# Performance work log

Hardware: AMD Instinct MI355X
Metric: run time of the kernel (lower is better)

## Reference

```python
import jax, jax.numpy as jnp
import numpy as np

BETA = 0.25  # commitment weight from __init__ default
K, D = 512, 64


def setup_inputs() -> dict:
    key = jax.random.key(0)
    k1, k2 = jax.random.split(key)
    latents = jax.random.normal(k1, (32, 64, 64, 64), dtype=jnp.float32)  # [B, D, H, W]
    # nn.Embedding weight initialized uniform(-1/K, 1/K)
    emb_weight = jax.random.uniform(k2, (K, D), dtype=jnp.float32, minval=-1.0 / K, maxval=1.0 / K)
    return {"latents": latents, "emb_weight": emb_weight, "validation": 1}


def reference(latents, emb_weight, validation):
    B, Dc, H, W = latents.shape
    lat = jnp.transpose(latents, (0, 2, 3, 1))          # [B, H, W, D]
    flat = lat.reshape(-1, Dc)                           # [N, D]
    # pairwise squared distances via sum-of-squares + matmul (as in source)
    dist = (jnp.sum(flat * flat, axis=1, keepdims=True)
            + jnp.sum(emb_weight * emb_weight, axis=1)
            - 2.0 * flat @ emb_weight.T)                 # [N, K]
    inds = jnp.argmin(dist, axis=1)                      # [N]
    # one_hot @ emb_weight == gather
    q = emb_weight[inds].reshape(B, H, W, Dc)            # [B, H, W, D]
    commitment_loss = jnp.mean((jax.lax.stop_gradient(q) - lat) ** 2)
    embedding_loss = jnp.mean((q - jax.lax.stop_gradient(lat)) ** 2)
    # eloss starts at 0.0 (and stays 0 in validation), so topology terms vanish
    vq_loss = commitment_loss * BETA + embedding_loss
    # straight-through estimator
    q_st = lat + jax.lax.stop_gradient(q - lat)
    return jnp.transpose(q_st, (0, 3, 1, 2)), vq_loss
```

## Files before the change

### kernel.cpp

```cpp
#include <hip/hip_runtime.h>


typedef __bf16 bf16_t;
typedef __attribute__((ext_vector_type(8))) __bf16 bf16x8;
typedef __attribute__((ext_vector_type(16))) float floatx16;
typedef __attribute__((ext_vector_type(4))) float floatx4;

namespace {
constexpr int K    = 512;
constexpr int D    = 64;
constexpr int HW   = 4096;
constexpr int NPIX = 32 * HW;
constexpr int QOUT = NPIX * D;
constexpr int ROWB = 144;
constexpr int EXT_BYTES  = K * ROWB;
constexpr int BIAS_OFF   = EXT_BYTES;
constexpr int SMEM_BYTES = EXT_BYTES + K * 4;
constexpr int SMEM_CHUNKS = SMEM_BYTES / 1024;
}

__global__ __launch_bounds__(64) void vq_prep(const float* __restrict__ emb,
                                              char* __restrict__ ws,
                                              float* __restrict__ loss) {
    int k = blockIdx.x * 64 + threadIdx.x;
    if (k == 0) *loss = 0.0f;
    if (k >= K) return;
    const float4* row = (const float4*)(emb + k * D);
    float4 v[16];
#pragma unroll
    for (int i = 0; i < 16; ++i) v[i] = row[i];
    float s = 0.0f;
#pragma unroll
    for (int i = 0; i < 16; ++i)
        s += v[i].x * v[i].x + v[i].y * v[i].y + v[i].z * v[i].z + v[i].w * v[i].w;
    bf16_t r[72];
#pragma unroll
    for (int i = 0; i < 16; ++i) {
        r[4 * i + 0] = (bf16_t)v[i].x;
        r[4 * i + 1] = (bf16_t)v[i].y;
        r[4 * i + 2] = (bf16_t)v[i].z;
        r[4 * i + 3] = (bf16_t)v[i].w;
    }
#pragma unroll
    for (int i = 64; i < 72; ++i) r[i] = (bf16_t)0.0f;
    bf16_t* dst = (bf16_t*)(ws + (size_t)k * ROWB);
#pragma unroll
    for (int i = 0; i < 9; ++i)
        ((bf16x8*)dst)[i] = *(const bf16x8*)(r + 8 * i);
    ((float*)(ws + BIAS_OFF))[k] = 1.0f - 0.5f * s;
}

__global__ __launch_bounds__(512) void vq_mfma(
    const float* __restrict__ lat,
    const float* __restrict__ emb,
    const char* __restrict__ wsrc,
    float* __restrict__ out,
    float* __restrict__ loss) {
    __shared__ char smem[SMEM_BYTES];

    const int lane = threadIdx.x & 63;
    const int wave = threadIdx.x >> 6;
    const int col  = lane & 31;
    const int half = lane >> 5;
    const unsigned h4 = (unsigned)(half << 2);

    for (int c = wave; c < SMEM_CHUNKS; c += 8) {
        __builtin_amdgcn_global_load_lds(
            (const __attribute__((address_space(1))) unsigned int*)(wsrc + c * 1024 + lane * 16),
            (__attribute__((address_space(3))) unsigned int*)(smem + c * 1024),
            16, 0, 0);
    }
    __syncthreads();

    const int w  = blockIdx.x * 8 + wave;
    const int n0 = w * 64 + 2 * col;
    const int b  = n0 >> 12;
    const int hw = n0 & (HW - 1);
    const float* latp = lat + (size_t)b * D * HW + hw;

    float2 raw[32];
#pragma unroll
    for (int s = 0; s < 4; ++s)
#pragma unroll
        for (int j = 0; j < 8; ++j) {
            int d = s * 16 + half * 8 + j;
            raw[s * 8 + j] = *(const float2*)(latp + (size_t)d * HW);
        }

    bf16x8 bf[2][4];
    float xsq0 = 0.0f, xsq1 = 0.0f;
#pragma unroll
    for (int s = 0; s < 4; ++s)
#pragma unroll
        for (int j = 0; j < 8; ++j) {
            float2 v = raw[s * 8 + j];
            bf[0][s][j] = (bf16_t)v.x;
            bf[1][s][j] = (bf16_t)v.y;
            xsq0 += v.x * v.x;
            xsq1 += v.y * v.y;
        }

    unsigned best0 = 0u, best1 = 0u;
#pragma unroll 2
    for (int t = 0; t < 16; ++t) {
        floatx4 bi[4];
#pragma unroll
        for (int c4 = 0; c4 < 4; ++c4)
            bi[c4] = *(const floatx4*)(smem + BIAS_OFF + t * 128 + half * 16 + c4 * 32);
        floatx16 acc0, acc1;
#pragma unroll
        for (int r = 0; r < 16; ++r) {
            float bv = bi[r >> 2][r & 3];
            acc0[r] = bv;
            acc1[r] = bv;
        }
        const char* arow = smem + (size_t)(t * 32 + col) * ROWB + half * 16;
        bf16x8 af[4];
#pragma unroll
        for (int s = 0; s < 4; ++s) af[s] = *(const bf16x8*)(arow + s * 32);
#pragma unroll
        for (int s = 0; s < 4; ++s) {
            acc0 = __builtin_amdgcn_mfma_f32_32x32x16_bf16(af[s], bf[0][s], acc0, 0, 0, 0);
            acc1 = __builtin_amdgcn_mfma_f32_32x32x16_bf16(af[s], bf[1][s], acc1, 0, 0, 0);
        }
#pragma unroll
        for (int r = 0; r < 16; ++r) {
            unsigned cb = (unsigned)(t * 32 + ((r & 3) + 8 * (r >> 2))) | h4;
            unsigned c0 = (__float_as_uint(acc0[r]) & 0xFFFFFE00u) | cb;
            unsigned c1 = (__float_as_uint(acc1[r]) & 0xFFFFFE00u) | cb;
            best0 = best0 > c0 ? best0 : c0;
            best1 = best1 > c1 ? best1 : c1;
        }
    }
    {
        unsigned o0 = (unsigned)__shfl_xor((int)best0, 32, 64);
        unsigned o1 = (unsigned)__shfl_xor((int)best1, 32, 64);
        best0 = best0 > o0 ? best0 : o0;
        best1 = best1 > o1 ? best1 : o1;
    }
    const int k0 = (int)(best0 & 511u);
    const int k1 = (int)(best1 & 511u);
    const float sc0 = __uint_as_float(best0 & 0xFFFFFE00u);
    const float sc1 = __uint_as_float(best1 & 0xFFFFFE00u);

    const float* e0 = emb + k0 * D + half * 8;
    const float* e1 = emb + k1 * D + half * 8;
    float* outp = out + (size_t)b * D * HW + hw;
#pragma unroll
    for (int s = 0; s < 4; ++s) {
#pragma unroll
        for (int jh = 0; jh < 2; ++jh) {
            float4 a0 = *(const float4*)(e0 + s * 16 + jh * 4);
            float4 a1 = *(const float4*)(e1 + s * 16 + jh * 4);
            int dbase = s * 16 + half * 8 + jh * 4;
            *(float2*)(outp + (size_t)(dbase + 0) * HW) = make_float2(a0.x, a1.x);
            *(float2*)(outp + (size_t)(dbase + 1) * HW) = make_float2(a0.y, a1.y);
            *(float2*)(outp + (size_t)(dbase + 2) * HW) = make_float2(a0.z, a1.z);
            *(float2*)(outp + (size_t)(dbase + 3) * HW) = make_float2(a0.w, a1.w);
        }
    }

    float xsq0f = xsq0 + __shfl_xor(xsq0, 32, 64);
    float xsq1f = xsq1 + __shfl_xor(xsq1, 32, 64);
    float sqtot = (xsq0f - 2.0f * (sc0 - 1.0f)) + (xsq1f - 2.0f * (sc1 - 1.0f));
    sqtot *= 0.5f;

#pragma unroll
    for (int off = 32; off > 0; off >>= 1) sqtot += __shfl_down(sqtot, off, 64);
    __shared__ float part[8];
    if (lane == 0) part[wave] = sqtot;
    __syncthreads();
    if (threadIdx.x == 0) {
        float t = 0.0f;
#pragma unroll
        for (int i = 0; i < 8; ++i) t += part[i];
        atomicAdd(loss, t * (1.25f / (float)QOUT));
    }
}

extern "C" void kernel_launch(void* const* d_in, const int* in_sizes, int n_in,
                              void* d_out, int out_size, void* d_ws, size_t ws_size,
                              hipStream_t stream) {
    const float* lat = (const float*)d_in[0];
    const float* emb = (const float*)d_in[1];
    float* out       = (float*)d_out;
    float* loss      = out + QOUT;
    char* ws         = (char*)d_ws;

    vq_prep<<<K / 64, 64, 0, stream>>>(emb, ws, loss);
    vq_mfma<<<NPIX / 512, 512, 0, stream>>>(lat, emb, ws, out, loss);
}
```

Before: 100.4 us.

## Fuse codebook preprocessing into main kernel, build bf16 codebook in LDS per block

Removes the separate prep kernel and instead has each 512-thread block read the fp32 codebook, compute row norms and bias, and write the bf16 padded codebook directly into shared memory. The codebook load is issued after the latent loads so the two can overlap. The loss reset moves to a memset, and launch bounds request two blocks per CU. This trades one kernel launch and a workspace round trip for redundant per-block codebook conversion work (256 blocks each redo the conversion).

```diff
diff --git a/kernel.cpp b/kernel.cpp
--- a/kernel.cpp
+++ b/kernel.cpp
@@ -16,44 +16,11 @@
 constexpr int EXT_BYTES  = K * ROWB;
 constexpr int BIAS_OFF   = EXT_BYTES;
 constexpr int SMEM_BYTES = EXT_BYTES + K * 4;
-constexpr int SMEM_CHUNKS = SMEM_BYTES / 1024;
 }
 
-__global__ __launch_bounds__(64) void vq_prep(const float* __restrict__ emb,
-                                              char* __restrict__ ws,
-                                              float* __restrict__ loss) {
-    int k = blockIdx.x * 64 + threadIdx.x;
-    if (k == 0) *loss = 0.0f;
-    if (k >= K) return;
-    const float4* row = (const float4*)(emb + k * D);
-    float4 v[16];
-#pragma unroll
-    for (int i = 0; i < 16; ++i) v[i] = row[i];
-    float s = 0.0f;
-#pragma unroll
-    for (int i = 0; i < 16; ++i)
-        s += v[i].x * v[i].x + v[i].y * v[i].y + v[i].z * v[i].z + v[i].w * v[i].w;
-    bf16_t r[72];
-#pragma unroll
-    for (int i = 0; i < 16; ++i) {
-        r[4 * i + 0] = (bf16_t)v[i].x;
-        r[4 * i + 1] = (bf16_t)v[i].y;
-        r[4 * i + 2] = (bf16_t)v[i].z;
-        r[4 * i + 3] = (bf16_t)v[i].w;
-    }
-#pragma unroll
-    for (int i = 64; i < 72; ++i) r[i] = (bf16_t)0.0f;
-    bf16_t* dst = (bf16_t*)(ws + (size_t)k * ROWB);
-#pragma unroll
-    for (int i = 0; i < 9; ++i)
-        ((bf16x8*)dst)[i] = *(const bf16x8*)(r + 8 * i);
-    ((float*)(ws + BIAS_OFF))[k] = 1.0f - 0.5f * s;
-}
-
-__global__ __launch_bounds__(512) void vq_mfma(
+__global__ __launch_bounds__(512, 2) void vq_mfma(
     const float* __restrict__ lat,
     const float* __restrict__ emb,
-    const char* __restrict__ wsrc,
     float* __restrict__ out,
     float* __restrict__ loss) {
     __shared__ char smem[SMEM_BYTES];
@@ -63,14 +30,6 @@
     const int col  = lane & 31;
     const int half = lane >> 5;
     const unsigned h4 = (unsigned)(half << 2);
-
-    for (int c = wave; c < SMEM_CHUNKS; c += 8) {
-        __builtin_amdgcn_global_load_lds(
-            (const __attribute__((address_space(1))) unsigned int*)(wsrc + c * 1024 + lane * 16),
-            (__attribute__((address_space(3))) unsigned int*)(smem + c * 1024),
-            16, 0, 0);
-    }
-    __syncthreads();
 
     const int w  = blockIdx.x * 8 + wave;
     const int n0 = w * 64 + 2 * col;
@@ -86,6 +45,33 @@
             int d = s * 16 + half * 8 + j;
             raw[s * 8 + j] = *(const float2*)(latp + (size_t)d * HW);
         }
+
+    {
+        const int k = threadIdx.x;
+        const float4* row = (const float4*)(emb + (size_t)k * D);
+        char* dst = smem + (size_t)k * ROWB;
+        float s = 0.0f;
+#pragma unroll
+        for (int h = 0; h < 2; ++h) {
+            float4 v[8];
+#pragma unroll
+            for (int i = 0; i < 8; ++i) v[i] = row[h * 8 + i];
+#pragma unroll
+            for (int i = 0; i < 8; ++i)
+                s += v[i].x * v[i].x + v[i].y * v[i].y + v[i].z * v[i].z + v[i].w * v[i].w;
+#pragma unroll
+            for (int c = 0; c < 4; ++c) {
+                bf16x8 p;
+                p[0] = (bf16_t)v[2 * c].x;     p[1] = (bf16_t)v[2 * c].y;
+                p[2] = (bf16_t)v[2 * c].z;     p[3] = (bf16_t)v[2 * c].w;
+                p[4] = (bf16_t)v[2 * c + 1].x; p[5] = (bf16_t)v[2 * c + 1].y;
+                p[6] = (bf16_t)v[2 * c + 1].z; p[7] = (bf16_t)v[2 * c + 1].w;
+                *(bf16x8*)(dst + (h * 4 + c) * 16) = p;
+            }
+        }
+        ((float*)(smem + BIAS_OFF))[k] = 1.0f - 0.5f * s;
+    }
+    __syncthreads();
 
     bf16x8 bf[2][4];
     float xsq0 = 0.0f, xsq1 = 0.0f;
@@ -185,8 +171,8 @@
     const float* emb = (const float*)d_in[1];
     float* out       = (float*)d_out;
     float* loss      = out + QOUT;
-    char* ws         = (char*)d_ws;
+    (void)d_ws; (void)ws_size;
 
-    vq_prep<<<K / 64, 64, 0, stream>>>(emb, ws, loss);
-    vq_mfma<<<NPIX / 512, 512, 0, stream>>>(lat, emb, ws, out, loss);
+    hipMemsetAsync(loss, 0, sizeof(float), stream);
+    vq_mfma<<<NPIX / 512, 512, 0, stream>>>(lat, emb, out, loss);
 }
```

After: 103.4 us. 3.0% more time.

## Split pixel pairs into two sequential halves to overlap loads, MFMA and stores

Applied to the files above, without the earlier changes.

Each wave now handles two groups of 32 contiguous pixels one after the other instead of interleaved float2 pixel pairs. The first group's latent loads are issued before the codebook LDS fill, and the second group's loads and the first group's stores overlap the MFMA loops. The argmin now uses fmaxf on float-encoded keys, and launch bounds request 2 blocks per SM to cap register use. The trade-off is scalar rather than float2 global accesses and a serialized dependency chain, with the occupancy cap possibly forcing spills.

```diff
diff --git a/kernel.cpp b/kernel.cpp
--- a/kernel.cpp
+++ b/kernel.cpp
@@ -50,7 +50,7 @@
     ((float*)(ws + BIAS_OFF))[k] = 1.0f - 0.5f * s;
 }
 
-__global__ __launch_bounds__(512) void vq_mfma(
+__global__ __launch_bounds__(512, 2) void vq_mfma(
     const float* __restrict__ lat,
     const float* __restrict__ emb,
     const char* __restrict__ wsrc,
@@ -62,7 +62,22 @@
     const int wave = threadIdx.x >> 6;
     const int col  = lane & 31;
     const int half = lane >> 5;
-    const unsigned h4 = (unsigned)(half << 2);
+
+    const int w  = blockIdx.x * 8 + wave;
+    const int nA = w * 64 + col;
+    const int b  = nA >> 12;
+    const int hwA = nA & (HW - 1);
+    const float* latpA = lat + (size_t)b * D * HW + hwA;
+    const float* latpB = latpA + 32;
+
+    float rA[32];
+#pragma unroll
+    for (int s = 0; s < 4; ++s)
+#pragma unroll
+        for (int j = 0; j < 8; ++j) {
+            int d = s * 16 + half * 8 + j;
+            rA[s * 8 + j] = latpA[(size_t)d * HW];
+        }
 
     for (int c = wave; c < SMEM_CHUNKS; c += 8) {
         __builtin_amdgcn_global_load_lds(
@@ -72,97 +87,120 @@
     }
     __syncthreads();
 
-    const int w  = blockIdx.x * 8 + wave;
-    const int n0 = w * 64 + 2 * col;
-    const int b  = n0 >> 12;
-    const int hw = n0 & (HW - 1);
-    const float* latp = lat + (size_t)b * D * HW + hw;
-
-    float2 raw[32];
+    bf16x8 bfA[4];
+    float xsqA = 0.0f;
+#pragma unroll
+    for (int s = 0; s < 4; ++s)
+#pragma unroll
+        for (int j = 0; j < 8; ++j) {
+            float v = rA[s * 8 + j];
+            bfA[s][j] = (bf16_t)v;
+            xsqA += v * v;
+        }
+
+    float rB[32];
 #pragma unroll
     for (int s = 0; s < 4; ++s)
 #pragma unroll
         for (int j = 0; j < 8; ++j) {
             int d = s * 16 + half * 8 + j;
-            raw[s * 8 + j] = *(const float2*)(latp + (size_t)d * HW);
-        }
-
-    bf16x8 bf[2][4];
-    float xsq0 = 0.0f, xsq1 = 0.0f;
-#pragma unroll
-    for (int s = 0; s < 4; ++s)
-#pragma unroll
-        for (int j = 0; j < 8; ++j) {
-            float2 v = raw[s * 8 + j];
-            bf[0][s][j] = (bf16_t)v.x;
-            bf[1][s][j] = (bf16_t)v.y;
-            xsq0 += v.x * v.x;
-            xsq1 += v.y * v.y;
-        }
-
-    unsigned best0 = 0u, best1 = 0u;
+            rB[s * 8 + j] = latpB[(size_t)d * HW];
+        }
+
+    auto tloop = [&](const bf16x8 (&bf)[4], float& bestf) {
 #pragma unroll 2
-    for (int t = 0; t < 16; ++t) {
-        floatx4 bi[4];
-#pragma unroll
-        for (int c4 = 0; c4 < 4; ++c4)
-            bi[c4] = *(const floatx4*)(smem + BIAS_OFF + t * 128 + half * 16 + c4 * 32);
-        floatx16 acc0, acc1;
-#pragma unroll
-        for (int r = 0; r < 16; ++r) {
-            float bv = bi[r >> 2][r & 3];
-            acc0[r] = bv;
-            acc1[r] = bv;
-        }
-        const char* arow = smem + (size_t)(t * 32 + col) * ROWB + half * 16;
-        bf16x8 af[4];
-#pragma unroll
-        for (int s = 0; s < 4; ++s) af[s] = *(const bf16x8*)(arow + s * 32);
-#pragma unroll
-        for (int s = 0; s < 4; ++s) {
-            acc0 = __builtin_amdgcn_mfma_f32_32x32x16_bf16(af[s], bf[0][s], acc0, 0, 0, 0);
-            acc1 = __builtin_amdgcn_mfma_f32_32x32x16_bf16(af[s], bf[1][s], acc1, 0, 0, 0);
-        }
-#pragma unroll
-        for (int r = 0; r < 16; ++r) {
-            unsigned cb = (unsigned)(t * 32 + ((r & 3) + 8 * (r >> 2))) | h4;
-            unsigned c0 = (__float_as_uint(acc0[r]) & 0xFFFFFE00u) | cb;
-            unsigned c1 = (__float_as_uint(acc1[r]) & 0xFFFFFE00u) | cb;
-            best0 = best0 > c0 ? best0 : c0;
-            best1 = best1 > c1 ? best1 : c1;
-        }
-    }
-    {
-        unsigned o0 = (unsigned)__shfl_xor((int)best0, 32, 64);
-        unsigned o1 = (unsigned)__shfl_xor((int)best1, 32, 64);
-        best0 = best0 > o0 ? best0 : o0;
-        best1 = best1 > o1 ? best1 : o1;
-    }
-    const int k0 = (int)(best0 & 511u);
-    const int k1 = (int)(best1 & 511u);
-    const float sc0 = __uint_as_float(best0 & 0xFFFFFE00u);
-    const float sc1 = __uint_as_float(best1 & 0xFFFFFE00u);
-
-    const float* e0 = emb + k0 * D + half * 8;
-    const float* e1 = emb + k1 * D + half * 8;
-    float* outp = out + (size_t)b * D * HW + hw;
+        for (int t = 0; t < 16; ++t) {
+            floatx4 bi[4];
+#pragma unroll
+            for (int c4 = 0; c4 < 4; ++c4)
+                bi[c4] = *(const floatx4*)(smem + BIAS_OFF + t * 128 + half * 16 + c4 * 32);
+            floatx16 acc;
+#pragma unroll
+            for (int r = 0; r < 16; ++r) acc[r] = bi[r >> 2][r & 3];
+            const char* arow = smem + (size_t)(t * 32 + col) * ROWB + half * 16;
+            bf16x8 af[4];
+#pragma unroll
+            for (int s = 0; s < 4; ++s) af[s] = *(const bf16x8*)(arow + s * 32);
+#pragma unroll
+            for (int s = 0; s < 4; ++s)
+                acc = __builtin_amdgcn_mfma_f32_32x32x16_bf16(af[s], bf[s], acc, 0, 0, 0);
+#pragma unroll
+            for (int r = 0; r < 16; r += 2) {
+                unsigned cb0 = (unsigned)(t * 32 + ((r & 3) + 8 * (r >> 2)));
+                unsigned cb1 = (unsigned)(t * 32 + (((r + 1) & 3) + 8 * ((r + 1) >> 2)));
+                float c0 = __uint_as_float((__float_as_uint(acc[r]) & 0xFFFFFE00u) | cb0);
+                float c1 = __uint_as_float((__float_as_uint(acc[r + 1]) & 0xFFFFFE00u) | cb1);
+                bestf = fmaxf(fmaxf(c0, c1), bestf);
+            }
+        }
+    };
+    auto resolve = [&](float bestf, int& kk, float& sc) {
+        float ob = __shfl_xor(bestf, 32, 64);
+        int oth = (half == 0) ? (ob >= bestf) : (ob > bestf);
+        float bw = fmaxf(ob, bestf);
+        unsigned bits = __float_as_uint(bw);
+        kk = (int)((bits & 511u) | (unsigned)((half ^ oth) << 2));
+        sc = __uint_as_float(bits & 0xFFFFFE00u);
+    };
+
+    float bestA = 0.0f;
+    tloop(bfA, bestA);
+    int kA; float scA;
+    resolve(bestA, kA, scA);
+
+    const float* eA = emb + kA * D + half * 8;
+    float4 qA[8];
 #pragma unroll
     for (int s = 0; s < 4; ++s) {
-#pragma unroll
-        for (int jh = 0; jh < 2; ++jh) {
-            float4 a0 = *(const float4*)(e0 + s * 16 + jh * 4);
-            float4 a1 = *(const float4*)(e1 + s * 16 + jh * 4);
-            int dbase = s * 16 + half * 8 + jh * 4;
-            *(float2*)(outp + (size_t)(dbase + 0) * HW) = make_float2(a0.x, a1.x);
-            *(float2*)(outp + (size_t)(dbase + 1) * HW) = make_float2(a0.y, a1.y);
-            *(float2*)(outp + (size_t)(dbase + 2) * HW) = make_float2(a0.z, a1.z);
-            *(float2*)(outp + (size_t)(dbase + 3) * HW) = make_float2(a0.w, a1.w);
-        }
-    }
-
-    float xsq0f = xsq0 + __shfl_xor(xsq0, 32, 64);
-    float xsq1f = xsq1 + __shfl_xor(xsq1, 32, 64);
-    float sqtot = (xsq0f - 2.0f * (sc0 - 1.0f)) + (xsq1f - 2.0f * (sc1 - 1.0f));
+        qA[2 * s]     = *(const float4*)(eA + s * 16);
+        qA[2 * s + 1] = *(const float4*)(eA + s * 16 + 4);
+    }
+
+    bf16x8 bfB[4];
+    float xsqB = 0.0f;
+#pragma unroll
+    for (int s = 0; s < 4; ++s)
+#pragma unroll
+        for (int j = 0; j < 8; ++j) {
+            float v = rB[s * 8 + j];
+            bfB[s][j] = (bf16_t)v;
+            xsqB += v * v;
+        }
+
+    float* outpA = out + (size_t)b * D * HW + hwA;
+#pragma unroll
+    for (int s = 0; s < 4; ++s)
+#pragma unroll
+        for (int j = 0; j < 8; ++j) {
+            int d = s * 16 + half * 8 + j;
+            outpA[(size_t)d * HW] = qA[2 * s + (j >> 2)][j & 3];
+        }
+
+    float bestB = 0.0f;
+    tloop(bfB, bestB);
+    int kB; float scB;
+    resolve(bestB, kB, scB);
+
+    const float* eB = emb + kB * D + half * 8;
+    float* outpB = outpA + 32;
+#pragma unroll
+    for (int s = 0; s < 4; ++s) {
+        float4 q0 = *(const float4*)(eB + s * 16);
+        float4 q1 = *(const float4*)(eB + s * 16 + 4);
+        int dbase = s * 16 + half * 8;
+        outpB[(size_t)(dbase + 0) * HW] = q0.x;
+        outpB[(size_t)(dbase + 1) * HW] = q0.y;
+        outpB[(size_t)(dbase + 2) * HW] = q0.z;
+        outpB[(size_t)(dbase + 3) * HW] = q0.w;
+        outpB[(size_t)(dbase + 4) * HW] = q1.x;
+        outpB[(size_t)(dbase + 5) * HW] = q1.y;
+        outpB[(size_t)(dbase + 6) * HW] = q1.z;
+        outpB[(size_t)(dbase + 7) * HW] = q1.w;
+    }
+
+    float xsqAf = xsqA + __shfl_xor(xsqA, 32, 64);
+    float xsqBf = xsqB + __shfl_xor(xsqB, 32, 64);
+    float sqtot = (xsqAf - 2.0f * (scA - 1.0f)) + (xsqBf - 2.0f * (scB - 1.0f));
     sqtot *= 0.5f;
 
 #pragma unroll
```

Result: no change. 99.85 us (-0.6%).
